# Performance work log

Measured on AMD Instinct MI355X. Metric: run time of the kernel, lower is better.

The kernel has to match this reference:

```python
import jax, jax.numpy as jnp
import numpy as np

GRID_SIZE = 5
SPLINE_ORDER = 3
GRID_LO, GRID_HI = -1.0, 1.0
N_BASIS = GRID_SIZE + SPLINE_ORDER  # 8


def make_grid():
    # Extended knot vector as in efficient-kan: grid_size+2*spline_order+1 points
    h = (GRID_HI - GRID_LO) / GRID_SIZE
    return (jnp.arange(-SPLINE_ORDER, GRID_SIZE + SPLINE_ORDER + 1, dtype=jnp.float32) * h + GRID_LO)  # (12,)


def b_splines(x, grid):
    # Cox-de Boor recursion; x: (...,) -> (..., N_BASIS)
    xg = x[..., None]
    bases = ((xg >= grid[:-1]) & (xg < grid[1:])).astype(x.dtype)
    for k in range(1, SPLINE_ORDER + 1):
        left = (xg - grid[: -(k + 1)]) / (grid[k:-1] - grid[: -(k + 1)]) * bases[..., :-1]
        right = (grid[k + 1:] - xg) / (grid[k + 1:] - grid[1:-k]) * bases[..., 1:]
        bases = left + right
    return bases


def extract_patches3(x):
    # x: (B, C, H, W) -> (B, C, 9, H, W); 3x3 kernel, stride 1, padding 1
    B, C, H, W = x.shape
    xp = jnp.pad(x, ((0, 0), (0, 0), (1, 1), (1, 1)))
    return jnp.stack([xp[:, :, di:di + H, dj:dj + W]
                      for di in range(3) for dj in range(3)], axis=2)


def kan_conv(x, base_w, spline_w, scaler, grid):
    # One KANLinear(9 -> 1) per (out_ch, in_ch) pair, summed over in_ch.
    p = extract_patches3(x)                          # (B, Cin, 9, H, W)
    base = jnp.einsum('biphw,oip->bohw', jax.nn.silu(p), base_w)
    basis = b_splines(p, grid)                       # (B, Cin, 9, H, W, G)
    sw = spline_w * scaler[..., None]                # standalone spline scaler
    spl = jnp.einsum('biphwg,oipg->bohw', basis, sw)
    return base + spl


def maxpool2(x):
    B, C, H, W = x.shape
    return x.reshape(B, C, H // 2, 2, W // 2, 2).max(axis=(3, 5))


def setup_inputs() -> dict:
    key = jax.random.key(0)
    ks = jax.random.split(key, 7)
    return {
        'x': jax.random.normal(ks[0], (2048, 1, 28, 28), dtype=jnp.float32),
        'base_w1': jax.random.normal(ks[1], (2, 1, 9), dtype=jnp.float32) * 0.3,
        'spline_w1': jax.random.normal(ks[2], (2, 1, 9, 8), dtype=jnp.float32) * 0.1,
        'scaler1': jax.random.normal(ks[3], (2, 1, 9), dtype=jnp.float32) * 0.3 + 1.0,
        'base_w2': jax.random.normal(ks[4], (2, 2, 9), dtype=jnp.float32) * 0.3,
        'spline_w2': jax.random.normal(ks[5], (2, 2, 9, 8), dtype=jnp.float32) * 0.1,
        'scaler2': jax.random.normal(ks[6], (2, 2, 9), dtype=jnp.float32) * 0.3 + 1.0,
    }


def reference(x, base_w1, spline_w1, scaler1, base_w2, spline_w2, scaler2):
    grid = make_grid()
    h = maxpool2(kan_conv(x, base_w1, spline_w1, scaler1, grid))   # (B, 2, 14, 14)
    h = maxpool2(kan_conv(h, base_w2, spline_w2, scaler2, grid))   # (B, 2, 7, 7)
    return h.reshape(h.shape[0], -1)                               # (B, 98)
```

## Files before the change

kernel.cpp:

```cpp
#include <hip/hip_runtime.h>
#include <math.h>

typedef _Float16 half_t;
typedef _Float16 h2 __attribute__((ext_vector_type(2)));
typedef unsigned int uint;
typedef unsigned long long u64;

#define TPB 256

__device__ __forceinline__ uint pack_h2f(float a, float b) {
  half_t ha = (half_t)a, hb = (half_t)b;
  unsigned short ua = __builtin_bit_cast(unsigned short, ha);
  unsigned short ub = __builtin_bit_cast(unsigned short, hb);
  return (uint)ua | ((uint)ub << 16);
}

__device__ __forceinline__ float silu_f(float x) {
  float e = __expf(-x);
  return x * __builtin_amdgcn_rcpf(1.0f + e);
}

__device__ __forceinline__ float dot8(uint d0, uint d1, uint d2, uint d3,
                                      float sv, const uint* __restrict__ w,
                                      float acc) {
  acc = fmaf(sv, __uint_as_float(w[4]), acc);
#if __has_builtin(__builtin_amdgcn_fdot2)
  acc = __builtin_amdgcn_fdot2(__builtin_bit_cast(h2, d0), __builtin_bit_cast(h2, w[0]), acc, false);
  acc = __builtin_amdgcn_fdot2(__builtin_bit_cast(h2, d1), __builtin_bit_cast(h2, w[1]), acc, false);
  acc = __builtin_amdgcn_fdot2(__builtin_bit_cast(h2, d2), __builtin_bit_cast(h2, w[2]), acc, false);
  acc = __builtin_amdgcn_fdot2(__builtin_bit_cast(h2, d3), __builtin_bit_cast(h2, w[3]), acc, false);
#else
  uint dd[4] = {d0, d1, d2, d3};
#pragma unroll
  for (int k = 0; k < 4; ++k) {
    h2 f = __builtin_bit_cast(h2, dd[k]);
    h2 wv = __builtin_bit_cast(h2, w[k]);
    acc = fmaf((float)f.x, (float)wv.x, acc);
    acc = fmaf((float)f.y, (float)wv.y, acc);
  }
#endif
  return acc;
}

__device__ __forceinline__ uint4 make_basis(float x) {
  float s = fmaf(x, 2.5f, 5.5f);
  float sf = floorf(s);
  float t = s - sf;
  int p = (int)sf - 3;
  float omt = 1.0f - t, t2 = t * t;
  float B0 = (1.0f / 6.0f) * omt * omt * omt;
  float B3 = (1.0f / 6.0f) * t2 * t;
  float B1 = fmaf(0.5f * t, t2, 2.0f / 3.0f - t2);
  float B2 = 1.0f - B0 - B1 - B3;
  u64 A = ((u64)pack_h2f(B2, B3) << 32) | pack_h2f(B0, B1);
  int n = p < 0 ? -p : 0;
  A = (n >= 4) ? 0ull : (A >> (16 * n));
  int pc = p < 0 ? 0 : (p > 9 ? 9 : p);
  int sh = 16 * pc;
  u64 lo = (sh < 64) ? (A << sh) : 0ull;
  u64 hi = (sh == 0) ? 0ull
         : (sh < 64) ? (A >> (64 - sh))
         : (sh < 128) ? (A << (sh - 64)) : 0ull;
  return make_uint4((uint)lo, (uint)(lo >> 32), (uint)hi, (uint)(hi >> 32));
}

__global__ void pack_w(const float* __restrict__ bw1, const float* __restrict__ sw1,
                       const float* __restrict__ sc1, const float* __restrict__ bw2,
                       const float* __restrict__ sw2, const float* __restrict__ sc2,
                       uint* __restrict__ W) {
  const int t = threadIdx.x;
  if (t < 18) {
    const float scv = sc1[t];
    uint* dst = W + t * 5;
#pragma unroll
    for (int j = 0; j < 4; ++j)
      dst[j] = pack_h2f(sw1[t * 8 + 2 * j] * scv, sw1[t * 8 + 2 * j + 1] * scv);
    dst[4] = __float_as_uint(bw1[t]);
  } else if (t < 54) {
    const int q = t - 18;
    const float scv = sc2[q];
    uint* dst = W + 90 + q * 5;
#pragma unroll
    for (int j = 0; j < 4; ++j)
      dst[j] = pack_h2f(sw2[q * 8 + 2 * j] * scv, sw2[q * 8 + 2 * j + 1] * scv);
    dst[4] = __float_as_uint(bw2[q]);
  }
}

#define F2DB 3600
#define F2SB 5168

__global__ __launch_bounds__(TPB, 5) void kan_fwd(
    const float* __restrict__ x, const uint* __restrict__ W,
    float* __restrict__ out)
{
  __shared__ __align__(16) uint lds[5560];
  float* P = (float*)lds;

  const int tid = threadIdx.x;
  const float* xb = x + (size_t)blockIdx.x * 784;

  for (int ii = tid; ii < 900; ii += TPB) {
    int r = ii / 30, c = ii % 30;
    bool inter = ((uint)(r - 1) < 28u) && ((uint)(c - 1) < 28u);
    int xi = (r - 1) * 28 + (c - 1);
    xi = min(max(xi, 0), 783);
    float xv = xb[xi];
    xv = inter ? xv : 0.0f;
    uint4 bs = make_basis(xv);
    *(uint4*)&lds[ii * 4] = bs;
  }
  __syncthreads();

  if (tid < 196) {
    const int ph = tid / 14, pw = tid % 14;
    float xv[16];
#pragma unroll
    for (int r = 0; r < 4; ++r) {
      int ir = 2 * ph + r - 1;
#pragma unroll
      for (int c = 0; c < 4; ++c) {
        int ic = 2 * pw + c - 1;
        bool ok = ((uint)ir < 28u) && ((uint)ic < 28u);
        int xi = min(max(ir * 28 + ic, 0), 783);
        float v = xb[xi];
        xv[r * 4 + c] = ok ? v : 0.0f;
      }
    }
    float acc[2][4];
#pragma unroll
    for (int o = 0; o < 2; ++o)
#pragma unroll
      for (int q = 0; q < 4; ++q) acc[o][q] = 0.0f;
#pragma unroll
    for (int r = 0; r < 4; ++r) {
#pragma unroll
      for (int c = 0; c < 4; ++c) {
        const uint4 fr = *(const uint4*)&lds[((2 * ph + r) * 30 + (2 * pw + c)) * 4];
        const float sv = silu_f(xv[r * 4 + c]);
#pragma unroll
        for (int dh = 0; dh < 2; ++dh) {
          if (r - dh < 0 || r - dh > 2) continue;
#pragma unroll
          for (int dw = 0; dw < 2; ++dw) {
            if (c - dw < 0 || c - dw > 2) continue;
            const int tap = (r - dh) * 3 + (c - dw);
#pragma unroll
            for (int o = 0; o < 2; ++o)
              acc[o][dh * 2 + dw] =
                  dot8(fr.x, fr.y, fr.z, fr.w, sv, W + (o * 9 + tap) * 5, acc[o][dh * 2 + dw]);
          }
        }
      }
    }
#pragma unroll
    for (int o = 0; o < 2; ++o) {
      float m = fmaxf(fmaxf(acc[o][0], acc[o][1]), fmaxf(acc[o][2], acc[o][3]));
      const int fi = o * 196 + tid;
      uint4 bm = make_basis(m);
      *(uint4*)&lds[F2DB + fi * 4] = bm;
      lds[F2SB + fi] = __float_as_uint(silu_f(m));
    }
  }
  __syncthreads();

  {
    const int wid = __builtin_amdgcn_readfirstlane(tid >> 6);
    const int lane = tid & 63;
    const uint F0d1 = pack_h2f(1.0f / 48.0f, 23.0f / 48.0f);
    const uint F0d2 = pack_h2f(23.0f / 48.0f, 1.0f / 48.0f);
    if (lane < 49) {
      const int ci = wid & 1;
      const int ph = lane / 7, pw = lane % 7;
      float pa[4] = {0.0f, 0.0f, 0.0f, 0.0f};
#pragma unroll
      for (int r = 0; r < 4; ++r) {
#pragma unroll
        for (int c = 0; c < 4; ++c) {
          int row = 2 * ph + r - 1, col = 2 * pw + c - 1;
          bool ok = ((uint)row < 14u) && ((uint)col < 14u);
          int rcl = min(max(row, 0), 13), ccl = min(max(col, 0), 13);
          const int idx = ci * 196 + rcl * 14 + ccl;
          const uint4 d = *(const uint4*)&lds[F2DB + idx * 4];
          float sv = __uint_as_float(lds[F2SB + idx]);
          sv = ok ? sv : 0.0f;
          uint d0 = ok ? d.x : 0u;
          uint d1 = ok ? d.y : F0d1;
          uint d2 = ok ? d.z : F0d2;
          uint d3 = ok ? d.w : 0u;
#pragma unroll
          for (int dh = 0; dh < 2; ++dh) {
            if (r - dh < 0 || r - dh > 2) continue;
#pragma unroll
            for (int dw = 0; dw < 2; ++dw) {
              if (c - dw < 0 || c - dw > 2) continue;
              const int tap = (r - dh) * 3 + (c - dw);
              pa[dh * 2 + dw] =
                  dot8(d0, d1, d2, d3, sv, W + 90 + (wid * 9 + tap) * 5, pa[dh * 2 + dw]);
            }
          }
        }
      }
      *(float4*)&P[(wid * 49 + lane) * 4] = make_float4(pa[0], pa[1], pa[2], pa[3]);
    }
  }
  __syncthreads();

  if (tid < 98) {
    const int o = tid / 49, pos = tid % 49;
    const float4 p0 = *(const float4*)&P[((o * 2 + 0) * 49 + pos) * 4];
    const float4 p1 = *(const float4*)&P[((o * 2 + 1) * 49 + pos) * 4];
    float m = fmaxf(fmaxf(p0.x + p1.x, p0.y + p1.y), fmaxf(p0.z + p1.z, p0.w + p1.w));
    out[(size_t)blockIdx.x * 98 + tid] = m;
  }
}

extern "C" void kernel_launch(void* const* d_in, const int* in_sizes, int n_in,
                              void* d_out, int out_size, void* d_ws, size_t ws_size,
                              hipStream_t stream) {
  const float* x   = (const float*)d_in[0];
  const float* bw1 = (const float*)d_in[1];
  const float* sw1 = (const float*)d_in[2];
  const float* sc1 = (const float*)d_in[3];
  const float* bw2 = (const float*)d_in[4];
  const float* sw2 = (const float*)d_in[5];
  const float* sc2 = (const float*)d_in[6];
  float* out = (float*)d_out;
  uint* W = (uint*)d_ws;
  const int B = in_sizes[0] / 784;
  pack_w<<<1, 64, 0, stream>>>(bw1, sw1, sc1, bw2, sw2, sc2, W);
  kan_fwd<<<B, TPB, 0, stream>>>(x, W, out);
}
```

Measured before the change: 85.86 us.

## Restructure KAN conv kernel into a single-wavefront block per image

Each block now uses one 64-thread wavefront per image instead of 256 threads. The first layer loops over 196 pooled outputs in four passes. The second layer computes both output channels and sums both input channels within one lane, so the partial-sum LDS buffer and one barrier go away. The padded 30x30 basis tile becomes an unpadded 28x28 tile with boundary handling in registers, and the layer-2 silu values are stored in fp16 to shrink LDS. The tradeoff is more serial work per lane, 49 of 64 lanes active in layer 2, and reliance on many small blocks to keep occupancy up.

```diff
diff --git a/kernel.cpp b/kernel.cpp
--- a/kernel.cpp
+++ b/kernel.cpp
@@ -6,7 +6,7 @@
 typedef unsigned int uint;
 typedef unsigned long long u64;
 
-#define TPB 256
+#define TPB 64
 
 __device__ __forceinline__ uint pack_h2f(float a, float b) {
   half_t ha = (half_t)a, hb = (half_t)b;
@@ -87,131 +87,127 @@
   }
 }
 
-#define F2DB 3600
-#define F2SB 5168
-
-__global__ __launch_bounds__(TPB, 5) void kan_fwd(
+#define F2DB 3136
+#define F2SB 4704
+
+__global__ __launch_bounds__(TPB, 2) void kan_fwd(
     const float* __restrict__ x, const uint* __restrict__ W,
     float* __restrict__ out)
 {
-  __shared__ __align__(16) uint lds[5560];
-  float* P = (float*)lds;
-
-  const int tid = threadIdx.x;
+  __shared__ __align__(16) uint lds[4900];
+  half_t* F2S = (half_t*)&lds[F2SB];
+
+  const int lane = threadIdx.x;
   const float* xb = x + (size_t)blockIdx.x * 784;
 
-  for (int ii = tid; ii < 900; ii += TPB) {
-    int r = ii / 30, c = ii % 30;
-    bool inter = ((uint)(r - 1) < 28u) && ((uint)(c - 1) < 28u);
-    int xi = (r - 1) * 28 + (c - 1);
-    xi = min(max(xi, 0), 783);
-    float xv = xb[xi];
-    xv = inter ? xv : 0.0f;
-    uint4 bs = make_basis(xv);
-    *(uint4*)&lds[ii * 4] = bs;
+  const uint F0d1 = pack_h2f(1.0f / 48.0f, 23.0f / 48.0f);
+  const uint F0d2 = pack_h2f(23.0f / 48.0f, 1.0f / 48.0f);
+
+  for (int s = lane; s < 784; s += TPB) {
+    uint4 bs = make_basis(xb[s]);
+    *(uint4*)&lds[s * 4] = bs;
   }
   __syncthreads();
 
-  if (tid < 196) {
-    const int ph = tid / 14, pw = tid % 14;
-    float xv[16];
-#pragma unroll
-    for (int r = 0; r < 4; ++r) {
-      int ir = 2 * ph + r - 1;
-#pragma unroll
-      for (int c = 0; c < 4; ++c) {
-        int ic = 2 * pw + c - 1;
-        bool ok = ((uint)ir < 28u) && ((uint)ic < 28u);
-        int xi = min(max(ir * 28 + ic, 0), 783);
-        float v = xb[xi];
-        xv[r * 4 + c] = ok ? v : 0.0f;
+  for (int k = 0; k < 4; ++k) {
+    const int q = lane + 64 * k;
+    if (q < 196) {
+      const int ph = q / 14, pw = q - (q / 14) * 14;
+      float acc[2][4];
+#pragma unroll
+      for (int o = 0; o < 2; ++o)
+#pragma unroll
+        for (int j = 0; j < 4; ++j) acc[o][j] = 0.0f;
+#pragma unroll
+      for (int r = 0; r < 4; ++r) {
+        const int ir = 2 * ph + r - 1;
+#pragma unroll
+        for (int c = 0; c < 4; ++c) {
+          const int ic = 2 * pw + c - 1;
+          const bool ok = ((uint)ir < 28u) && ((uint)ic < 28u);
+          const int idx = min(max(ir * 28 + ic, 0), 783);
+          float xv = xb[idx];
+          const float sv = ok ? silu_f(xv) : 0.0f;
+          const uint4 d = *(const uint4*)&lds[idx * 4];
+          const uint d0 = ok ? d.x : 0u;
+          const uint d1 = ok ? d.y : F0d1;
+          const uint d2 = ok ? d.z : F0d2;
+          const uint d3 = ok ? d.w : 0u;
+#pragma unroll
+          for (int dh = 0; dh < 2; ++dh) {
+            if (r - dh < 0 || r - dh > 2) continue;
+#pragma unroll
+            for (int dw = 0; dw < 2; ++dw) {
+              if (c - dw < 0 || c - dw > 2) continue;
+              const int tap = (r - dh) * 3 + (c - dw);
+#pragma unroll
+              for (int o = 0; o < 2; ++o)
+                acc[o][dh * 2 + dw] =
+                    dot8(d0, d1, d2, d3, sv, W + (o * 9 + tap) * 5, acc[o][dh * 2 + dw]);
+            }
+          }
+        }
+      }
+#pragma unroll
+      for (int o = 0; o < 2; ++o) {
+        const float m = fmaxf(fmaxf(acc[o][0], acc[o][1]), fmaxf(acc[o][2], acc[o][3]));
+        const int fi = o * 196 + q;
+        uint4 bm = make_basis(m);
+        *(uint4*)&lds[F2DB + fi * 4] = bm;
+        F2S[fi] = (half_t)silu_f(m);
       }
     }
-    float acc[2][4];
+  }
+  __syncthreads();
+
+  if (lane < 49) {
+    const int ph = lane / 7, pw = lane - (lane / 7) * 7;
+    float pa[2][4];
 #pragma unroll
     for (int o = 0; o < 2; ++o)
 #pragma unroll
-      for (int q = 0; q < 4; ++q) acc[o][q] = 0.0f;
-#pragma unroll
-    for (int r = 0; r < 4; ++r) {
-#pragma unroll
-      for (int c = 0; c < 4; ++c) {
-        const uint4 fr = *(const uint4*)&lds[((2 * ph + r) * 30 + (2 * pw + c)) * 4];
-        const float sv = silu_f(xv[r * 4 + c]);
-#pragma unroll
-        for (int dh = 0; dh < 2; ++dh) {
-          if (r - dh < 0 || r - dh > 2) continue;
-#pragma unroll
-          for (int dw = 0; dw < 2; ++dw) {
-            if (c - dw < 0 || c - dw > 2) continue;
-            const int tap = (r - dh) * 3 + (c - dw);
-#pragma unroll
-            for (int o = 0; o < 2; ++o)
-              acc[o][dh * 2 + dw] =
-                  dot8(fr.x, fr.y, fr.z, fr.w, sv, W + (o * 9 + tap) * 5, acc[o][dh * 2 + dw]);
+      for (int j = 0; j < 4; ++j) pa[o][j] = 0.0f;
+#pragma unroll
+    for (int ci = 0; ci < 2; ++ci) {
+#pragma unroll
+      for (int r = 0; r < 4; ++r) {
+        const int row = 2 * ph + r - 1;
+        const int rcl = min(max(row, 0), 13);
+#pragma unroll
+        for (int c = 0; c < 4; ++c) {
+          const int col = 2 * pw + c - 1;
+          const bool ok = ((uint)row < 14u) && ((uint)col < 14u);
+          const int ccl = min(max(col, 0), 13);
+          const int idx = ci * 196 + rcl * 14 + ccl;
+          const uint4 d = *(const uint4*)&lds[F2DB + idx * 4];
+          float sv = (float)F2S[idx];
+          sv = ok ? sv : 0.0f;
+          const uint d0 = ok ? d.x : 0u;
+          const uint d1 = ok ? d.y : F0d1;
+          const uint d2 = ok ? d.z : F0d2;
+          const uint d3 = ok ? d.w : 0u;
+#pragma unroll
+          for (int dh = 0; dh < 2; ++dh) {
+            if (r - dh < 0 || r - dh > 2) continue;
+#pragma unroll
+            for (int dw = 0; dw < 2; ++dw) {
+              if (c - dw < 0 || c - dw > 2) continue;
+              const int tap = (r - dh) * 3 + (c - dw);
+#pragma unroll
+              for (int o = 0; o < 2; ++o)
+                pa[o][dh * 2 + dw] =
+                    dot8(d0, d1, d2, d3, sv,
+                         W + 90 + ((o * 2 + ci) * 9 + tap) * 5, pa[o][dh * 2 + dw]);
+            }
           }
         }
       }
     }
 #pragma unroll
     for (int o = 0; o < 2; ++o) {
-      float m = fmaxf(fmaxf(acc[o][0], acc[o][1]), fmaxf(acc[o][2], acc[o][3]));
-      const int fi = o * 196 + tid;
-      uint4 bm = make_basis(m);
-      *(uint4*)&lds[F2DB + fi * 4] = bm;
-      lds[F2SB + fi] = __float_as_uint(silu_f(m));
+      const float m = fmaxf(fmaxf(pa[o][0], pa[o][1]), fmaxf(pa[o][2], pa[o][3]));
+      out[(size_t)blockIdx.x * 98 + o * 49 + lane] = m;
     }
-  }
-  __syncthreads();
-
-  {
-    const int wid = __builtin_amdgcn_readfirstlane(tid >> 6);
-    const int lane = tid & 63;
-    const uint F0d1 = pack_h2f(1.0f / 48.0f, 23.0f / 48.0f);
-    const uint F0d2 = pack_h2f(23.0f / 48.0f, 1.0f / 48.0f);
-    if (lane < 49) {
-      const int ci = wid & 1;
-      const int ph = lane / 7, pw = lane % 7;
-      float pa[4] = {0.0f, 0.0f, 0.0f, 0.0f};
-#pragma unroll
-      for (int r = 0; r < 4; ++r) {
-#pragma unroll
-        for (int c = 0; c < 4; ++c) {
-          int row = 2 * ph + r - 1, col = 2 * pw + c - 1;
-          bool ok = ((uint)row < 14u) && ((uint)col < 14u);
-          int rcl = min(max(row, 0), 13), ccl = min(max(col, 0), 13);
-          const int idx = ci * 196 + rcl * 14 + ccl;
-          const uint4 d = *(const uint4*)&lds[F2DB + idx * 4];
-          float sv = __uint_as_float(lds[F2SB + idx]);
-          sv = ok ? sv : 0.0f;
-          uint d0 = ok ? d.x : 0u;
-          uint d1 = ok ? d.y : F0d1;
-          uint d2 = ok ? d.z : F0d2;
-          uint d3 = ok ? d.w : 0u;
-#pragma unroll
-          for (int dh = 0; dh < 2; ++dh) {
-            if (r - dh < 0 || r - dh > 2) continue;
-#pragma unroll
-            for (int dw = 0; dw < 2; ++dw) {
-              if (c - dw < 0 || c - dw > 2) continue;
-              const int tap = (r - dh) * 3 + (c - dw);
-              pa[dh * 2 + dw] =
-                  dot8(d0, d1, d2, d3, sv, W + 90 + (wid * 9 + tap) * 5, pa[dh * 2 + dw]);
-            }
-          }
-        }
-      }
-      *(float4*)&P[(wid * 49 + lane) * 4] = make_float4(pa[0], pa[1], pa[2], pa[3]);
-    }
-  }
-  __syncthreads();
-
-  if (tid < 98) {
-    const int o = tid / 49, pos = tid % 49;
-    const float4 p0 = *(const float4*)&P[((o * 2 + 0) * 49 + pos) * 4];
-    const float4 p1 = *(const float4*)&P[((o * 2 + 1) * 49 + pos) * 4];
-    float m = fmaxf(fmaxf(p0.x + p1.x, p0.y + p1.y), fmaxf(p0.z + p1.z, p0.w + p1.w));
-    out[(size_t)blockIdx.x * 98 + tid] = m;
   }
 }
 
```

Result: slower. 97.09 us (+13.1%).
